# Kernel optimization log

Hardware: AMD Instinct MI355X
Metric: run time of the kernel (lower is better)

The kernel has to match this reference:

```python
import jax, jax.numpy as jnp
import numpy as np

BITS = 12
MB = BITS - 1                      # mantissa bits
MAX_VAL = 1.0 - 2.0 ** (-MB)       # superfloat max representable magnitude
DENOM = float(2 ** MB - 1)


def sf_decode(enc):
    # enc: int32. NOTE: faithful to source, including its sign convention
    # decoded * (2*sign - 1) where sign=1 for negative inputs (flips sign).
    mantissa = enc & ((1 << MB) - 1)
    sign = (enc >> MB) & 1
    mag = mantissa.astype(jnp.float32) / DENOM * MAX_VAL
    return mag * (2 * sign - 1).astype(jnp.float32)


def sf_encode(x):
    c = jnp.clip(x, -MAX_VAL, MAX_VAL)
    oor = jnp.abs(x) > MAX_VAL
    mantissa = jnp.floor(jnp.abs(c) * DENOM / MAX_VAL).astype(jnp.int32)
    sign = (c < 0).astype(jnp.int32)
    return (mantissa | (sign << MB)), oor


def setup_inputs() -> dict:
    key = jax.random.key(0)
    k1, k2, k3, k4, k5 = jax.random.split(key, 5)
    T, IN, OUT = 512, 4096, 11008
    x = jax.random.normal(k1, (T, IN), dtype=jnp.float32)
    weight_full = jax.random.normal(k2, (OUT, IN), dtype=jnp.float32) * 0.02
    scale = jnp.ones((OUT,), dtype=jnp.float32)
    bias = jax.random.normal(k3, (OUT,), dtype=jnp.float32) * 0.01
    encoded_weight = jax.random.randint(k4, (OUT, IN), 0, 2 ** BITS, dtype=jnp.int32)
    outlier_mask = jax.random.uniform(k5, (OUT, IN)) < 0.005
    return {"x": x, "weight_full": weight_full, "scale": scale, "bias": bias,
            "encoded_weight": encoded_weight, "outlier_mask": outlier_mask}


def reference(x, weight_full, scale, bias, encoded_weight, outlier_mask):
    # decode packed superfloat weight, scatter outliers, rescale per-row
    w = sf_decode(encoded_weight)                       # [OUT, IN]
    w = jnp.where(outlier_mask, weight_full, w)         # == w[mask] = weight[mask]
    w = w * scale[:, None]
    # quantize activations (encode then decode)
    enc_x, _ = sf_encode(x)
    xq = sf_decode(enc_x)                               # [T, IN]
    return xq @ w.T + bias                              # [T, OUT]
```

## Files before the change

kernel.cpp:

```cpp
#include <hip/hip_runtime.h>
#include <hip/hip_bf16.h>
#include <stdint.h>

#define T_DIM 512
#define IN_DIM 4096
#define OUT_DIM 11008

#define BN 32
#define BK 64
#define KC 4
#define KCHUNK (IN_DIM / KC)
#define KSTEPS (KCHUNK / BK)
#define NBLK (OUT_DIM / BN)
#define PSZ ((size_t)T_DIM * OUT_DIM)

typedef __attribute__((ext_vector_type(8))) __bf16 bf16x8;
typedef __attribute__((ext_vector_type(8))) short shortx8;
typedef __attribute__((ext_vector_type(4))) float f32x4;
typedef __attribute__((ext_vector_type(4))) int   intx4;

__device__ __forceinline__ short f32_to_bf16_bits(float f) {
    uint32_t x = __builtin_bit_cast(uint32_t, f);
    x += 0x7FFFu + ((x >> 16) & 1u);
    return (short)(x >> 16);
}

__device__ __forceinline__ void bar_lgkm() {
    asm volatile("s_waitcnt lgkmcnt(0)" ::: "memory");
    __builtin_amdgcn_s_barrier();
}

__global__ __launch_bounds__(256) void encode_x_kernel(const float* __restrict__ x,
                                                       short* __restrict__ xq) {
    const float MAXV = 2047.0f / 2048.0f;
    int i = (blockIdx.x * 256 + threadIdx.x) * 8;
    float4 a = *(const float4*)(x + i);
    float4 b = *(const float4*)(x + i + 4);
    float v[8] = {a.x, a.y, a.z, a.w, b.x, b.y, b.z, b.w};
    union { short s[8]; int4 v4; } u;
#pragma unroll
    for (int j = 0; j < 8; ++j) {
        float xv = v[j];
        float ax = fminf(fabsf(xv), MAXV);
        float m = floorf(ax * 2047.0f / MAXV);
        float q = m * (1.0f / 2048.0f) * (xv < 0.0f ? 1.0f : -1.0f);
        u.s[j] = f32_to_bf16_bits(q);
    }
    *(int4*)(xq + i) = u.v4;
}

__global__ __launch_bounds__(512, 4) void fused_dq_gemm_kernel(
    const short* __restrict__ A,
    const int*   __restrict__ enc,
    const int*   __restrict__ mask,
    const float* __restrict__ wf,
    const float* __restrict__ scale,
    float*       __restrict__ Cp)
{
    __shared__ short Ws[2][BN * BK];

    const int tid  = threadIdx.x;
    const int wave = tid >> 6;
    const int lane = tid & 63;
    const int quad = lane >> 4;
    const int lr   = lane & 15;
    const int wm   = wave * 64;
    const int bn   = blockIdx.x;
    const int kc   = blockIdx.y;
    const int kbase = kc * KCHUNK;

    const int wrow = tid >> 4;
    const int q4   = tid & 15;
    const int grow = bn * BN + wrow;
    const float s     = scale[grow];
    const float s2048 = s * (1.0f / 2048.0f);
    const int*   ep = enc  + (size_t)grow * IN_DIM + kbase + q4 * 4;
    const int*   mp = mask + (size_t)grow * IN_DIM + kbase + q4 * 4;
    const float* wp = wf   + (size_t)grow * IN_DIM + kbase + q4 * 4;
    char* wsw_base = (char*)&Ws[0][0] +
        ((wrow * (BK * 2) + q4 * 8) ^ ((wrow & 7) << 4));

    const short* pa = A + (size_t)(wm + lr) * IN_DIM + kbase + quad * 8;

    f32x4 acc[4][2] = {};

    auto WS_FRAG = [&](int rb, int ni, int kf) -> bf16x8 {
        const int row  = ni * 16 + lr;
        const int byte = ((row * (BK * 2) + quad * 16 + kf * 64) ^ ((row & 7) << 4))
                         + rb * (BN * BK * 2);
        return __builtin_bit_cast(bf16x8, *(const shortx8*)((const char*)&Ws[0][0] + byte));
    };

    auto DQW = [&](const intx4 E, const int* mv, const float* wv, int wb) {
        union { short h[4]; int2 q2; } u;
#pragma unroll
        for (int j = 0; j < 4; ++j) {
            int ev = E[j];
            float d = (float)(ev & 2047);
            if (!(ev & 2048)) d = -d;
            float v = d * s2048;
            if (mv[j]) v = wv[j] * s;
            u.h[j] = f32_to_bf16_bits(v);
        }
        *(int2*)(wsw_base + wb * (BN * BK * 2)) = u.q2;
    };

    intx4 eA, mA, eB, mB;
    eA = __builtin_nontemporal_load((const intx4*)(ep));
    mA = __builtin_nontemporal_load((const intx4*)(mp));
    eB = __builtin_nontemporal_load((const intx4*)(ep + BK));
    mB = __builtin_nontemporal_load((const intx4*)(mp + BK));

    {
        int   mv0[4] = {mA[0], mA[1], mA[2], mA[3]};
        float wv0[4];
#pragma unroll
        for (int j = 0; j < 4; ++j)
            if (mv0[j]) wv0[j] = wp[j];
        DQW(eA, mv0, wv0, 0);
    }
    __syncthreads();

#define STEP(KT, Ei, Mi, Ed, Md, RB, WB)                                               \
    {                                                                                  \
        const int ko = (KT) * BK;                                                      \
        bf16x8 af[4][2];                                                               \
        _Pragma("unroll")                                                              \
        for (int mi = 0; mi < 4; ++mi) {                                               \
            const short* p = pa + (size_t)mi * (16 * IN_DIM) + ko;                     \
            af[mi][0] = __builtin_bit_cast(bf16x8, *(const shortx8*)(p));              \
            af[mi][1] = __builtin_bit_cast(bf16x8, *(const shortx8*)(p + 32));         \
        }                                                                              \
        if ((KT) + 2 < KSTEPS) {                                                       \
            Ei = __builtin_nontemporal_load((const intx4*)(ep + ko + 2 * BK));         \
            Mi = __builtin_nontemporal_load((const intx4*)(mp + ko + 2 * BK));         \
        }                                                                              \
        int mdv[4]; float wv[4];                                                       \
        if ((KT) + 1 < KSTEPS) {                                                       \
            mdv[0] = Md[0]; mdv[1] = Md[1]; mdv[2] = Md[2]; mdv[3] = Md[3];            \
            _Pragma("unroll")                                                          \
            for (int j = 0; j < 4; ++j)                                                \
                if (mdv[j]) wv[j] = wp[ko + BK + j];                                   \
        }                                                                              \
        _Pragma("unroll")                                                              \
        for (int kf = 0; kf < 2; ++kf) {                                               \
            bf16x8 b0 = WS_FRAG(RB, 0, kf);                                            \
            bf16x8 b1 = WS_FRAG(RB, 1, kf);                                            \
            _Pragma("unroll")                                                          \
            for (int mi = 0; mi < 4; ++mi) {                                           \
                acc[mi][0] = __builtin_amdgcn_mfma_f32_16x16x32_bf16(af[mi][kf], b0,   \
                                                                     acc[mi][0], 0, 0, 0); \
                acc[mi][1] = __builtin_amdgcn_mfma_f32_16x16x32_bf16(af[mi][kf], b1,   \
                                                                     acc[mi][1], 0, 0, 0); \
            }                                                                          \
        }                                                                              \
        if ((KT) + 1 < KSTEPS) DQW(Ed, mdv, wv, WB);                                   \
        bar_lgkm();                                                                    \
    }

    for (int kt = 0; kt < KSTEPS; kt += 2) {
        STEP(kt,     eA, mA, eB, mB, 0, 1)
        STEP(kt + 1, eB, mB, eA, mA, 1, 0)
    }
#undef STEP

    float* pc = Cp + (size_t)kc * PSZ;
    const int rowb = wm + quad * 4;
    const int colb = bn * BN + lr;
#pragma unroll
    for (int ni = 0; ni < 2; ++ni) {
        const int col = colb + ni * 16;
#pragma unroll
        for (int mi = 0; mi < 4; ++mi) {
#pragma unroll
            for (int r = 0; r < 4; ++r) {
                const int row = rowb + mi * 16 + r;
                pc[(size_t)row * OUT_DIM + col] = acc[mi][ni][r];
            }
        }
    }
}

__global__ __launch_bounds__(256) void reduce_kernel(const float* __restrict__ P,
                                                     const float* __restrict__ bias,
                                                     float* __restrict__ C) {
    size_t i = ((size_t)blockIdx.x * 256 + threadIdx.x) * 4;
    int col = (int)(i % OUT_DIM);
    float4 s0 = *(const float4*)(P + i);
    float4 s1 = *(const float4*)(P + PSZ + i);
    float4 s2 = *(const float4*)(P + 2 * PSZ + i);
    float4 s3 = *(const float4*)(P + 3 * PSZ + i);
    float4 b  = *(const float4*)(bias + col);
    float4 o;
    o.x = s0.x + s1.x + s2.x + s3.x + b.x;
    o.y = s0.y + s1.y + s2.y + s3.y + b.y;
    o.z = s0.z + s1.z + s2.z + s3.z + b.z;
    o.w = s0.w + s1.w + s2.w + s3.w + b.w;
    *(float4*)(C + i) = o;
}

extern "C" void kernel_launch(void* const* d_in, const int* in_sizes, int n_in,
                              void* d_out, int out_size, void* d_ws, size_t ws_size,
                              hipStream_t stream) {
    const float* x     = (const float*)d_in[0];
    const float* wfull = (const float*)d_in[1];
    const float* scale = (const float*)d_in[2];
    const float* bias  = (const float*)d_in[3];
    const int*   enc   = (const int*)d_in[4];
    const int*   mask  = (const int*)d_in[5];

    float* out = (float*)d_out;
    short* xq  = (short*)d_ws;
    float* Cp  = (float*)((char*)d_ws + (size_t)T_DIM * IN_DIM * 2);

    encode_x_kernel<<<(T_DIM * IN_DIM) / (256 * 8), 256, 0, stream>>>(x, xq);
    dim3 grid(NBLK, KC);
    fused_dq_gemm_kernel<<<grid, 512, 0, stream>>>(xq, enc, mask, wfull, scale, Cp);
    reduce_kernel<<<(int)(PSZ / (256 * 4)), 256, 0, stream>>>(Cp, bias, out);
}
```

Measured before the change: 577.5 us.

## Decode weights directly into registers with single-wave blocks, dropping LDS staging

Replaces the 512-thread block, which staged dequantized weights through double-buffered LDS with barriers, with one-wave blocks. Each lane decodes its own B-fragment straight from global memory into registers. The M dimension is split into two halves of 256 rows, so each weight element is now decoded twice, and each wave holds 32 accumulator tiles. This removes LDS traffic and barriers, but doubles the encoded-weight and mask reads, adds register pressure, and makes A-fragment loads uncoalesced global reads with no LDS reuse.

```diff
diff --git a/kernel.cpp b/kernel.cpp
--- a/kernel.cpp
+++ b/kernel.cpp
@@ -6,12 +6,10 @@
 #define IN_DIM 4096
 #define OUT_DIM 11008
 
-#define BN 32
-#define BK 64
+#define NW 32
+#define MH 256
 #define KC 4
 #define KCHUNK (IN_DIM / KC)
-#define KSTEPS (KCHUNK / BK)
-#define NBLK (OUT_DIM / BN)
 #define PSZ ((size_t)T_DIM * OUT_DIM)
 
 typedef __attribute__((ext_vector_type(8))) __bf16 bf16x8;
@@ -23,11 +21,6 @@
     uint32_t x = __builtin_bit_cast(uint32_t, f);
     x += 0x7FFFu + ((x >> 16) & 1u);
     return (short)(x >> 16);
-}
-
-__device__ __forceinline__ void bar_lgkm() {
-    asm volatile("s_waitcnt lgkmcnt(0)" ::: "memory");
-    __builtin_amdgcn_s_barrier();
 }
 
 __global__ __launch_bounds__(256) void encode_x_kernel(const float* __restrict__ x,
@@ -49,7 +42,7 @@
     *(int4*)(xq + i) = u.v4;
 }
 
-__global__ __launch_bounds__(512, 4) void fused_dq_gemm_kernel(
+__global__ __launch_bounds__(64, 2) void fused_dq_gemm_kernel(
     const short* __restrict__ A,
     const int*   __restrict__ enc,
     const int*   __restrict__ mask,
@@ -57,121 +50,106 @@
     const float* __restrict__ scale,
     float*       __restrict__ Cp)
 {
-    __shared__ short Ws[2][BN * BK];
-
-    const int tid  = threadIdx.x;
-    const int wave = tid >> 6;
-    const int lane = tid & 63;
+    const int lane = threadIdx.x;
     const int quad = lane >> 4;
     const int lr   = lane & 15;
-    const int wm   = wave * 64;
     const int bn   = blockIdx.x;
-    const int kc   = blockIdx.y;
-    const int kbase = kc * KCHUNK;
+    const int mh   = blockIdx.y;
+    const int kc   = blockIdx.z;
 
-    const int wrow = tid >> 4;
-    const int q4   = tid & 15;
-    const int grow = bn * BN + wrow;
-    const float s     = scale[grow];
-    const float s2048 = s * (1.0f / 2048.0f);
-    const int*   ep = enc  + (size_t)grow * IN_DIM + kbase + q4 * 4;
-    const int*   mp = mask + (size_t)grow * IN_DIM + kbase + q4 * 4;
-    const float* wp = wf   + (size_t)grow * IN_DIM + kbase + q4 * 4;
-    char* wsw_base = (char*)&Ws[0][0] +
-        ((wrow * (BK * 2) + q4 * 8) ^ ((wrow & 7) << 4));
+    const int gcol0 = bn * NW + lr;
+    const int gcol1 = gcol0 + 16;
+    const size_t kbase = (size_t)kc * KCHUNK;
 
-    const short* pa = A + (size_t)(wm + lr) * IN_DIM + kbase + quad * 8;
+    const float s0 = scale[gcol0], s1 = scale[gcol1];
+    const float t0 = s0 * (1.0f / 2048.0f);
+    const float t1 = s1 * (1.0f / 2048.0f);
 
-    f32x4 acc[4][2] = {};
+    const int*   ep0 = enc  + (size_t)gcol0 * IN_DIM + kbase + quad * 8;
+    const int*   ep1 = enc  + (size_t)gcol1 * IN_DIM + kbase + quad * 8;
+    const int*   mp0 = mask + (size_t)gcol0 * IN_DIM + kbase + quad * 8;
+    const int*   mp1 = mask + (size_t)gcol1 * IN_DIM + kbase + quad * 8;
+    const float* wp0 = wf   + (size_t)gcol0 * IN_DIM + kbase + quad * 8;
+    const float* wp1 = wf   + (size_t)gcol1 * IN_DIM + kbase + quad * 8;
 
-    auto WS_FRAG = [&](int rb, int ni, int kf) -> bf16x8 {
-        const int row  = ni * 16 + lr;
-        const int byte = ((row * (BK * 2) + quad * 16 + kf * 64) ^ ((row & 7) << 4))
-                         + rb * (BN * BK * 2);
-        return __builtin_bit_cast(bf16x8, *(const shortx8*)((const char*)&Ws[0][0] + byte));
+    const short* pa = A + (size_t)(mh * MH + lr) * IN_DIM + kbase + quad * 8;
+
+    f32x4 acc[16][2] = {};
+
+    auto DEC = [&](intx4 ea, intx4 eb, intx4 ma, intx4 mb,
+                   const float* wp, int ko, float sv, float tv) -> bf16x8 {
+        int ev[8] = {ea[0], ea[1], ea[2], ea[3], eb[0], eb[1], eb[2], eb[3]};
+        int mv[8] = {ma[0], ma[1], ma[2], ma[3], mb[0], mb[1], mb[2], mb[3]};
+        float wv[8];
+#pragma unroll
+        for (int j = 0; j < 8; ++j)
+            if (mv[j]) wv[j] = wp[ko + j];
+        union { short h[8]; shortx8 v; } u;
+#pragma unroll
+        for (int j = 0; j < 8; ++j) {
+            float d = (float)(ev[j] & 2047);
+            if (!(ev[j] & 2048)) d = -d;
+            float v = d * tv;
+            if (mv[j]) v = wv[j] * sv;
+            u.h[j] = f32_to_bf16_bits(v);
+        }
+        return __builtin_bit_cast(bf16x8, u.v);
     };
 
-    auto DQW = [&](const intx4 E, const int* mv, const float* wv, int wb) {
-        union { short h[4]; int2 q2; } u;
+    intx4 cE00 = *(const intx4*)(ep0);
+    intx4 cE01 = *(const intx4*)(ep0 + 4);
+    intx4 cE10 = *(const intx4*)(ep1);
+    intx4 cE11 = *(const intx4*)(ep1 + 4);
+    intx4 cM00 = *(const intx4*)(mp0);
+    intx4 cM01 = *(const intx4*)(mp0 + 4);
+    intx4 cM10 = *(const intx4*)(mp1);
+    intx4 cM11 = *(const intx4*)(mp1 + 4);
+
+    for (int ko = 0; ko < KCHUNK; ko += 32) {
+        intx4 nE00, nE01, nE10, nE11, nM00, nM01, nM10, nM11;
+        const bool more = (ko + 32) < KCHUNK;
+        if (more) {
+            nE00 = *(const intx4*)(ep0 + ko + 32);
+            nE01 = *(const intx4*)(ep0 + ko + 36);
+            nE10 = *(const intx4*)(ep1 + ko + 32);
+            nE11 = *(const intx4*)(ep1 + ko + 36);
+            nM00 = *(const intx4*)(mp0 + ko + 32);
+            nM01 = *(const intx4*)(mp0 + ko + 36);
+            nM10 = *(const intx4*)(mp1 + ko + 32);
+            nM11 = *(const intx4*)(mp1 + ko + 36);
+        }
+
+        bf16x8 b0 = DEC(cE00, cE01, cM00, cM01, wp0, ko, s0, t0);
+        bf16x8 b1 = DEC(cE10, cE11, cM10, cM11, wp1, ko, s1, t1);
+
 #pragma unroll
-        for (int j = 0; j < 4; ++j) {
-            int ev = E[j];
-            float d = (float)(ev & 2047);
-            if (!(ev & 2048)) d = -d;
-            float v = d * s2048;
-            if (mv[j]) v = wv[j] * s;
-            u.h[j] = f32_to_bf16_bits(v);
+        for (int mi = 0; mi < 8; ++mi) {
+            bf16x8 af = __builtin_bit_cast(bf16x8,
+                *(const shortx8*)(pa + (size_t)mi * (16 * IN_DIM) + ko));
+            acc[mi][0] = __builtin_amdgcn_mfma_f32_16x16x32_bf16(af, b0, acc[mi][0], 0, 0, 0);
+            acc[mi][1] = __builtin_amdgcn_mfma_f32_16x16x32_bf16(af, b1, acc[mi][1], 0, 0, 0);
         }
-        *(int2*)(wsw_base + wb * (BN * BK * 2)) = u.q2;
-    };
+#pragma unroll
+        for (int mi = 8; mi < 16; ++mi) {
+            bf16x8 af = __builtin_bit_cast(bf16x8,
+                *(const shortx8*)(pa + (size_t)mi * (16 * IN_DIM) + ko));
+            acc[mi][0] = __builtin_amdgcn_mfma_f32_16x16x32_bf16(af, b0, acc[mi][0], 0, 0, 0);
+            acc[mi][1] = __builtin_amdgcn_mfma_f32_16x16x32_bf16(af, b1, acc[mi][1], 0, 0, 0);
+        }
 
-    intx4 eA, mA, eB, mB;
-    eA = __builtin_nontemporal_load((const intx4*)(ep));
-    mA = __builtin_nontemporal_load((const intx4*)(mp));
-    eB = __builtin_nontemporal_load((const intx4*)(ep + BK));
-    mB = __builtin_nontemporal_load((const intx4*)(mp + BK));
-
-    {
-        int   mv0[4] = {mA[0], mA[1], mA[2], mA[3]};
-        float wv0[4];
-#pragma unroll
-        for (int j = 0; j < 4; ++j)
-            if (mv0[j]) wv0[j] = wp[j];
-        DQW(eA, mv0, wv0, 0);
-    }
-    __syncthreads();
-
-#define STEP(KT, Ei, Mi, Ed, Md, RB, WB)                                               \
-    {                                                                                  \
-        const int ko = (KT) * BK;                                                      \
-        bf16x8 af[4][2];                                                               \
-        _Pragma("unroll")                                                              \
-        for (int mi = 0; mi < 4; ++mi) {                                               \
-            const short* p = pa + (size_t)mi * (16 * IN_DIM) + ko;                     \
-            af[mi][0] = __builtin_bit_cast(bf16x8, *(const shortx8*)(p));              \
-            af[mi][1] = __builtin_bit_cast(bf16x8, *(const shortx8*)(p + 32));         \
-        }                                                                              \
-        if ((KT) + 2 < KSTEPS) {                                                       \
-            Ei = __builtin_nontemporal_load((const intx4*)(ep + ko + 2 * BK));         \
-            Mi = __builtin_nontemporal_load((const intx4*)(mp + ko + 2 * BK));         \
-        }                                                                              \
-        int mdv[4]; float wv[4];                                                       \
-        if ((KT) + 1 < KSTEPS) {                                                       \
-            mdv[0] = Md[0]; mdv[1] = Md[1]; mdv[2] = Md[2]; mdv[3] = Md[3];            \
-            _Pragma("unroll")                                                          \
-            for (int j = 0; j < 4; ++j)                                                \
-                if (mdv[j]) wv[j] = wp[ko + BK + j];                                   \
-        }                                                                              \
-        _Pragma("unroll")                                                              \
-        for (int kf = 0; kf < 2; ++kf) {                                               \
-            bf16x8 b0 = WS_FRAG(RB, 0, kf);                                            \
-            bf16x8 b1 = WS_FRAG(RB, 1, kf);                                            \
-            _Pragma("unroll")                                                          \
-            for (int mi = 0; mi < 4; ++mi) {                                           \
-                acc[mi][0] = __builtin_amdgcn_mfma_f32_16x16x32_bf16(af[mi][kf], b0,   \
-                                                                     acc[mi][0], 0, 0, 0); \
-                acc[mi][1] = __builtin_amdgcn_mfma_f32_16x16x32_bf16(af[mi][kf], b1,   \
-                                                                     acc[mi][1], 0, 0, 0); \
-            }                                                                          \
-        }                                                                              \
-        if ((KT) + 1 < KSTEPS) DQW(Ed, mdv, wv, WB);                                   \
-        bar_lgkm();                                                                    \
+        if (more) {
+            cE00 = nE00; cE01 = nE01; cE10 = nE10; cE11 = nE11;
+            cM00 = nM00; cM01 = nM01; cM10 = nM10; cM11 = nM11;
+        }
     }
 
-    for (int kt = 0; kt < KSTEPS; kt += 2) {
-        STEP(kt,     eA, mA, eB, mB, 0, 1)
-        STEP(kt + 1, eB, mB, eA, mA, 1, 0)
-    }
-#undef STEP
-
     float* pc = Cp + (size_t)kc * PSZ;
-    const int rowb = wm + quad * 4;
-    const int colb = bn * BN + lr;
+    const int rowb = mh * MH + quad * 4;
 #pragma unroll
     for (int ni = 0; ni < 2; ++ni) {
-        const int col = colb + ni * 16;
+        const int col = bn * NW + ni * 16 + lr;
 #pragma unroll
-        for (int mi = 0; mi < 4; ++mi) {
+        for (int mi = 0; mi < 16; ++mi) {
 #pragma unroll
             for (int r = 0; r < 4; ++r) {
                 const int row = rowb + mi * 16 + r;
@@ -214,7 +192,7 @@
     float* Cp  = (float*)((char*)d_ws + (size_t)T_DIM * IN_DIM * 2);
 
     encode_x_kernel<<<(T_DIM * IN_DIM) / (256 * 8), 256, 0, stream>>>(x, xq);
-    dim3 grid(NBLK, KC);
-    fused_dq_gemm_kernel<<<grid, 512, 0, stream>>>(xq, enc, mask, wfull, scale, Cp);
+    dim3 grid(OUT_DIM / NW, T_DIM / MH, KC);
+    fused_dq_gemm_kernel<<<grid, 64, 0, stream>>>(xq, enc, mask, wfull, scale, Cp);
     reduce_kernel<<<(int)(PSZ / (256 * 4)), 256, 0, stream>>>(Cp, bias, out);
 }
```

After: 732.2 us. +26.8%, slower.
